# Performance work log

Measured on AMD Instinct MI355X. Metric: run time of the kernel, lower is better.

Reference implementation:

```python
import jax, jax.numpy as jnp
import numpy as np

B = 8192
IN = 2048
H = 2048


def setup_inputs() -> dict:
    key = jax.random.key(0)
    ks = jax.random.split(key, 6)
    stdv = 1.0 / np.sqrt(H)
    return {
        "x": jax.random.normal(ks[0], (B, IN), dtype=jnp.float32),
        "h_prev": jax.random.normal(ks[1], (B, H), dtype=jnp.float32),
        "c_prev": jax.random.normal(ks[2], (B, H), dtype=jnp.float32),
        "weight_ih": jax.random.normal(ks[3], (4 * H, IN), dtype=jnp.float32) * stdv,
        "weight_hh": jax.random.normal(ks[4], (4 * H, H), dtype=jnp.float32) * stdv,
        "bias": jax.random.normal(ks[5], (4 * H,), dtype=jnp.float32) * stdv,
    }


def reference(x, h_prev, c_prev, weight_ih, weight_hh, bias):
    # gates: [B, 4H] = x @ W_ih^T + h_prev @ W_hh^T + b
    gates = x @ weight_ih.T + h_prev @ weight_hh.T + bias
    i, f, j, o = jnp.split(gates, 4, axis=1)
    i = jax.nn.sigmoid(i)
    f = jax.nn.sigmoid(f)
    o = jax.nn.sigmoid(o)
    j = jnp.tanh(j)
    # cap_input_gate=True: input gate capped by (1 - f)
    c = f * c_prev + jnp.minimum(1.0 - f, i) * j
    h = o * jnp.tanh(c)
    return (h, c)
```

## Files before the change

kernel.cpp:

```cpp
#include <hip/hip_runtime.h>

#define DEVI __device__ __forceinline__

typedef __attribute__((ext_vector_type(8))) __bf16 bf16x8;
typedef __attribute__((ext_vector_type(4))) float floatx4;

constexpr int Bsz = 8192;
constexpr int Hd  = 2048;
constexpr int INd = 2048;
constexpr int N1  = Bsz * INd;

DEVI unsigned short f2bf_rne(float f) {
  unsigned int u = __float_as_uint(f);
  u += 0x7FFFu + ((u >> 16) & 1u);
  return (unsigned short)(u >> 16);
}

__global__ void cvt4(const float* __restrict__ s0, const float* __restrict__ s1,
                     const float* __restrict__ s2, const float* __restrict__ s3,
                     unsigned short* __restrict__ dst) {
  const float* src = (blockIdx.y == 0) ? s0 : (blockIdx.y == 1) ? s1
                   : (blockIdx.y == 2) ? s2 : s3;
  unsigned short* out = dst + (size_t)blockIdx.y * N1;
  const int nv = N1 / 4;
  for (int i = blockIdx.x * blockDim.x + threadIdx.x; i < nv;
       i += gridDim.x * blockDim.x) {
    float4 v = ((const float4*)src)[i];
    ushort4 o;
    o.x = f2bf_rne(v.x); o.y = f2bf_rne(v.y);
    o.z = f2bf_rne(v.z); o.w = f2bf_rne(v.w);
    ((ushort4*)out)[i] = o;
  }
}

DEVI void gload_lds16(const void* g, void* l) {
  __builtin_amdgcn_global_load_lds(
      (const __attribute__((address_space(1))) void*)g,
      (__attribute__((address_space(3))) void*)l, 16, 0, 0);
}

DEVI float sigm(float x) { return 1.0f / (1.0f + __expf(-x)); }

__global__ __launch_bounds__(512, 2) void lstm_gemm(
    const unsigned short* __restrict__ ws,
    const float* __restrict__ bias,
    const float* __restrict__ c_prev,
    float* __restrict__ out_h,
    float* __restrict__ out_c) {
  __shared__ __align__(16) unsigned short sm[4 * 256 * 64];
  char* smc = (char*)sm;

  const unsigned short* xb  = ws;
  const unsigned short* hb  = ws + (size_t)N1;
  const unsigned short* wih = ws + (size_t)2 * N1;
  const unsigned short* whh = ws + (size_t)3 * N1;

  const int tid  = threadIdx.x;
  const int lane = tid & 63;
  const int wid  = tid >> 6;
  const int wm   = wid >> 2, wn = wid & 3;
  const int lr   = lane & 15, lk = lane >> 4;
  const int lr8  = lane >> 3;
  const int swc  = ((lane & 7) ^ lr8) * 8;

  const int wg = blockIdx.x;
  const int x8 = wg & 7;
  const int lc = wg >> 3;
  const int bc = (x8 & 3) * 8 + (lc & 7);
  const int rb = ((x8 >> 2) * 16 + (lc >> 3)) * 256;

  unsigned int aOff[2][2], bOff[2][2];
#pragma unroll
  for (int h = 0; h < 2; ++h)
#pragma unroll
    for (int j = 0; j < 2; ++j) {
      const int arow = rb + h * 128 + j * 64 + wid * 8 + lr8;
      aOff[h][j] = (unsigned)arow * 2048u + (unsigned)swc;
      const int c  = h * 128 + j * 64 + wid * 8 + lr8;
      const int cf = c >> 4, ce = c & 15;
      const int gate = (cf & 1) | ((cf >> 2) & 2);
      const int hch  = (cf >> 1) & 3;
      const int brow = gate * 2048 + bc * 64 + hch * 16 + ce;
      bOff[h][j] = (unsigned)brow * 2048u + (unsigned)swc;
    }

  floatx4 acc[2][4][2][2];
#pragma unroll
  for (int a = 0; a < 2; ++a)
#pragma unroll
    for (int b = 0; b < 4; ++b)
#pragma unroll
      for (int c = 0; c < 2; ++c)
#pragma unroll
        for (int d = 0; d < 2; ++d)
          acc[a][b][c][d] = (floatx4){0.f, 0.f, 0.f, 0.f};

#define STAGE_A(ts, h) {                                                      \
    const int bs_ = (ts) & 1;                                                 \
    const unsigned short* s_ = (((ts) < 32) ? xb : hb) + (((ts) & 31) * 64);  \
    gload_lds16(s_ + aOff[h][0], smc + bs_ * 32768 + ((h) * 128 + wid * 8) * 128);        \
    gload_lds16(s_ + aOff[h][1], smc + bs_ * 32768 + ((h) * 128 + 64 + wid * 8) * 128); }
#define STAGE_B(ts, h) {                                                      \
    const int bs_ = (ts) & 1;                                                 \
    const unsigned short* s_ = (((ts) < 32) ? wih : whh) + (((ts) & 31) * 64);\
    gload_lds16(s_ + bOff[h][0], smc + 65536 + bs_ * 32768 + ((h) * 128 + wid * 8) * 128);        \
    gload_lds16(s_ + bOff[h][1], smc + 65536 + bs_ * 32768 + ((h) * 128 + 64 + wid * 8) * 128); }

#define LDA(DST, QM)                                                          \
  _Pragma("unroll") for (int mr = 0; mr < 4; ++mr)                            \
    _Pragma("unroll") for (int s = 0; s < 2; ++s) {                           \
      const int row  = (QM) * 128 + wm * 64 + mr * 16 + lr;                   \
      const int phys = (s * 4 + lk) ^ (row & 7);                              \
      DST[mr][s] = *(const bf16x8*)(Ab + row * 128 + phys * 16); }
#define LDB(DST, QN)                                                          \
  _Pragma("unroll") for (int nc = 0; nc < 2; ++nc)                            \
    _Pragma("unroll") for (int s = 0; s < 2; ++s) {                           \
      const int row  = ((QN) * 8 + wn * 2 + nc) * 16 + lr;                    \
      const int phys = (s * 4 + lk) ^ (row & 7);                              \
      DST[nc][s] = *(const bf16x8*)(Bb + row * 128 + phys * 16); }
#define MFMA16(QM, QN, AF, BG)                                                \
  __builtin_amdgcn_s_setprio(1);                                              \
  _Pragma("unroll") for (int mr = 0; mr < 4; ++mr)                            \
    _Pragma("unroll") for (int nc = 0; nc < 2; ++nc)                          \
      _Pragma("unroll") for (int s = 0; s < 2; ++s)                           \
        acc[QM][mr][QN][nc] = __builtin_amdgcn_mfma_f32_16x16x32_bf16(        \
            AF[mr][s], BG[nc][s], acc[QM][mr][QN][nc], 0, 0, 0);              \
  __builtin_amdgcn_s_setprio(0);
#define BAR  asm volatile("s_barrier" ::: "memory")
#define LGK0 do { asm volatile("s_waitcnt lgkmcnt(0)" ::: "memory");          \
                  __builtin_amdgcn_sched_barrier(0); } while (0)

#define KTILE(BETA, S1, S2, S3, S4, W4) {                                     \
    const char* Ab = smc + (BETA) * 32768;                                    \
    const char* Bb = smc + 65536 + (BETA) * 32768;                            \
    bf16x8 afA[4][2], afB[4][2], bg[2][2];                                    \
    LDA(afA, 0); LDB(bg, 0); S1;                                              \
    asm volatile("s_waitcnt lgkmcnt(8)" ::: "memory");                        \
    BAR; LGK0; MFMA16(0, 0, afA, bg); BAR;                                    \
    LDA(afB, 1); S2;                                                          \
    BAR; LGK0; MFMA16(1, 0, afB, bg); BAR;                                    \
    LDB(bg, 1); S3;                                                           \
    BAR; LGK0; MFMA16(1, 1, afB, bg); BAR;                                    \
    LDA(afA, 0); S4; W4;                                                      \
    BAR; LGK0; MFMA16(0, 1, afA, bg); BAR;                                    \
  }
#define VM4  asm volatile("s_waitcnt vmcnt(4)" ::: "memory")
#define VM0  asm volatile("s_waitcnt vmcnt(0)" ::: "memory")
#define NOP  (void)0

  STAGE_B(0, 0); STAGE_A(0, 1); STAGE_B(0, 1);
  STAGE_A(0, 0); STAGE_B(1, 0); STAGE_A(1, 1);
  VM4;
  BAR;

  for (int t = 0; t < 62; ++t) {
    KTILE(t & 1, STAGE_B(t + 1, 1), STAGE_A(t + 1, 0),
          STAGE_B(t + 2, 0), STAGE_A(t + 2, 1), VM4);
  }
  KTILE(0, STAGE_B(63, 1), STAGE_A(63, 0), NOP, NOP, VM0);
  KTILE(1, NOP, NOP, NOP, NOP, NOP);

  const int hcol = bc * 64 + wn * 16 + lr;
  const float b_i = bias[hcol];
  const float b_f = bias[2048 + hcol];
  const float b_j = bias[4096 + hcol];
  const float b_o = bias[6144 + hcol];
#pragma unroll
  for (int qm = 0; qm < 2; ++qm)
#pragma unroll
    for (int mr = 0; mr < 4; ++mr)
#pragma unroll
      for (int r = 0; r < 4; ++r) {
        const int row = rb + qm * 128 + wm * 64 + mr * 16 + lk * 4 + r;
        const float gi = acc[qm][mr][0][0][r] + b_i;
        const float gf = acc[qm][mr][0][1][r] + b_f;
        const float gj = acc[qm][mr][1][0][r] + b_j;
        const float go = acc[qm][mr][1][1][r] + b_o;
        const float iv = sigm(gi);
        const float fv = sigm(gf);
        const float jv = tanhf(gj);
        const float ov = sigm(go);
        const size_t idx = (size_t)row * 2048 + hcol;
        const float cp = c_prev[idx];
        const float cv = fv * cp + fminf(1.0f - fv, iv) * jv;
        out_h[idx] = ov * tanhf(cv);
        out_c[idx] = cv;
      }
}

extern "C" void kernel_launch(void* const* d_in, const int* in_sizes, int n_in,
                              void* d_out, int out_size, void* d_ws, size_t ws_size,
                              hipStream_t stream) {
  const float* x      = (const float*)d_in[0];
  const float* h_prev = (const float*)d_in[1];
  const float* c_prev = (const float*)d_in[2];
  const float* w_ih   = (const float*)d_in[3];
  const float* w_hh   = (const float*)d_in[4];
  const float* bias   = (const float*)d_in[5];

  float* out_h = (float*)d_out;
  float* out_c = out_h + (size_t)Bsz * Hd;
  unsigned short* wsb = (unsigned short*)d_ws;

  dim3 cgrid(2048, 4);
  cvt4<<<cgrid, 256, 0, stream>>>(x, h_prev, w_ih, w_hh, wsb);

  lstm_gemm<<<1024, 512, 0, stream>>>(wsb, bias, c_prev, out_h, out_c);
}
```

Before: 599.8 us.

## Switch LSTM GEMM to 32x32x16 MFMA with swapped operands and vectorized epilogue

Replaces the 16x16x32 bf16 MFMA tiling with 32x32x16 MFMAs, with the weights as the A operand and activations as B. Weight rows are re-permuted so each lane's 16 accumulator outputs cover the i/f/j/o gates for 4 contiguous hidden columns. This allows float4 loads of bias and c_prev and float4 stores of h and c. The k-tile schedule is also simplified: the lgkmcnt waits and per-phase double barriers are dropped, which cuts sync overhead but relies on the compiler to insert correct LDS waits.

```diff
diff --git a/kernel.cpp b/kernel.cpp
--- a/kernel.cpp
+++ b/kernel.cpp
@@ -3,7 +3,7 @@
 #define DEVI __device__ __forceinline__
 
 typedef __attribute__((ext_vector_type(8))) __bf16 bf16x8;
-typedef __attribute__((ext_vector_type(4))) float floatx4;
+typedef __attribute__((ext_vector_type(16))) float floatx16;
 
 constexpr int Bsz = 8192;
 constexpr int Hd  = 2048;
@@ -58,8 +58,9 @@
   const int tid  = threadIdx.x;
   const int lane = tid & 63;
   const int wid  = tid >> 6;
-  const int wm   = wid >> 2, wn = wid & 3;
-  const int lr   = lane & 15, lk = lane >> 4;
+  const int ww   = wid >> 2;
+  const int wb   = wid & 3;
+  const int l31  = lane & 31, l5 = lane >> 5;
   const int lr8  = lane >> 3;
   const int swc  = ((lane & 7) ^ lr8) * 8;
 
@@ -76,24 +77,20 @@
     for (int j = 0; j < 2; ++j) {
       const int arow = rb + h * 128 + j * 64 + wid * 8 + lr8;
       aOff[h][j] = (unsigned)arow * 2048u + (unsigned)swc;
-      const int c  = h * 128 + j * 64 + wid * 8 + lr8;
-      const int cf = c >> 4, ce = c & 15;
-      const int gate = (cf & 1) | ((cf >> 2) & 2);
-      const int hch  = (cf >> 1) & 3;
-      const int brow = gate * 2048 + bc * 64 + hch * 16 + ce;
-      bOff[h][j] = (unsigned)brow * 2048u + (unsigned)swc;
+      const int wr = h * 128 + j * 64 + wid * 8 + lr8;
+      const int wrow = ((wr >> 3) & 3) * 2048 + bc * 64 + (wr >> 5) * 8 + (wr & 7);
+      bOff[h][j] = (unsigned)wrow * 2048u + (unsigned)swc;
     }
 
-  floatx4 acc[2][4][2][2];
+  floatx16 acc[2][2][2];
 #pragma unroll
   for (int a = 0; a < 2; ++a)
 #pragma unroll
-    for (int b = 0; b < 4; ++b)
+    for (int b = 0; b < 2; ++b)
 #pragma unroll
       for (int c = 0; c < 2; ++c)
 #pragma unroll
-        for (int d = 0; d < 2; ++d)
-          acc[a][b][c][d] = (floatx4){0.f, 0.f, 0.f, 0.f};
+        for (int e = 0; e < 16; ++e) acc[a][b][c][e] = 0.f;
 
 #define STAGE_A(ts, h) {                                                      \
     const int bs_ = (ts) & 1;                                                 \
@@ -106,86 +103,88 @@
     gload_lds16(s_ + bOff[h][0], smc + 65536 + bs_ * 32768 + ((h) * 128 + wid * 8) * 128);        \
     gload_lds16(s_ + bOff[h][1], smc + 65536 + bs_ * 32768 + ((h) * 128 + 64 + wid * 8) * 128); }
 
-#define LDA(DST, QM)                                                          \
-  _Pragma("unroll") for (int mr = 0; mr < 4; ++mr)                            \
-    _Pragma("unroll") for (int s = 0; s < 2; ++s) {                           \
-      const int row  = (QM) * 128 + wm * 64 + mr * 16 + lr;                   \
-      const int phys = (s * 4 + lk) ^ (row & 7);                              \
-      DST[mr][s] = *(const bf16x8*)(Ab + row * 128 + phys * 16); }
-#define LDB(DST, QN)                                                          \
-  _Pragma("unroll") for (int nc = 0; nc < 2; ++nc)                            \
-    _Pragma("unroll") for (int s = 0; s < 2; ++s) {                           \
-      const int row  = ((QN) * 8 + wn * 2 + nc) * 16 + lr;                    \
-      const int phys = (s * 4 + lk) ^ (row & 7);                              \
-      DST[nc][s] = *(const bf16x8*)(Bb + row * 128 + phys * 16); }
-#define MFMA16(QM, QN, AF, BG)                                                \
+#define LDW(DST, QW)                                                          \
+  _Pragma("unroll") for (int mrw = 0; mrw < 2; ++mrw)                         \
+    _Pragma("unroll") for (int ks = 0; ks < 4; ++ks) {                        \
+      const int row  = (QW) * 128 + ww * 64 + mrw * 32 + l31;                 \
+      const int phys = (ks * 2 + l5) ^ (row & 7);                             \
+      DST[mrw][ks] = *(const bf16x8*)(Bb + row * 128 + phys * 16); }
+#define LDX(DST, QB)                                                          \
+  _Pragma("unroll") for (int ks = 0; ks < 4; ++ks) {                          \
+      const int row  = (QB) * 128 + wb * 32 + l31;                            \
+      const int phys = (ks * 2 + l5) ^ (row & 7);                             \
+      DST[ks] = *(const bf16x8*)(Ab + row * 128 + phys * 16); }
+#define MM(QW, QB, WF, XF)                                                    \
   __builtin_amdgcn_s_setprio(1);                                              \
-  _Pragma("unroll") for (int mr = 0; mr < 4; ++mr)                            \
-    _Pragma("unroll") for (int nc = 0; nc < 2; ++nc)                          \
-      _Pragma("unroll") for (int s = 0; s < 2; ++s)                           \
-        acc[QM][mr][QN][nc] = __builtin_amdgcn_mfma_f32_16x16x32_bf16(        \
-            AF[mr][s], BG[nc][s], acc[QM][mr][QN][nc], 0, 0, 0);              \
+  _Pragma("unroll") for (int mrw = 0; mrw < 2; ++mrw)                         \
+    _Pragma("unroll") for (int ks = 0; ks < 4; ++ks)                          \
+      acc[QW][mrw][QB] = __builtin_amdgcn_mfma_f32_32x32x16_bf16(             \
+          WF[mrw][ks], XF[ks], acc[QW][mrw][QB], 0, 0, 0);                    \
   __builtin_amdgcn_s_setprio(0);
 #define BAR  asm volatile("s_barrier" ::: "memory")
-#define LGK0 do { asm volatile("s_waitcnt lgkmcnt(0)" ::: "memory");          \
-                  __builtin_amdgcn_sched_barrier(0); } while (0)
-
-#define KTILE(BETA, S1, S2, S3, S4, W4) {                                     \
-    const char* Ab = smc + (BETA) * 32768;                                    \
-    const char* Bb = smc + 65536 + (BETA) * 32768;                            \
-    bf16x8 afA[4][2], afB[4][2], bg[2][2];                                    \
-    LDA(afA, 0); LDB(bg, 0); S1;                                              \
-    asm volatile("s_waitcnt lgkmcnt(8)" ::: "memory");                        \
-    BAR; LGK0; MFMA16(0, 0, afA, bg); BAR;                                    \
-    LDA(afB, 1); S2;                                                          \
-    BAR; LGK0; MFMA16(1, 0, afB, bg); BAR;                                    \
-    LDB(bg, 1); S3;                                                           \
-    BAR; LGK0; MFMA16(1, 1, afB, bg); BAR;                                    \
-    LDA(afA, 0); S4; W4;                                                      \
-    BAR; LGK0; MFMA16(0, 1, afA, bg); BAR;                                    \
-  }
 #define VM4  asm volatile("s_waitcnt vmcnt(4)" ::: "memory")
 #define VM0  asm volatile("s_waitcnt vmcnt(0)" ::: "memory")
 #define NOP  (void)0
 
-  STAGE_B(0, 0); STAGE_A(0, 1); STAGE_B(0, 1);
-  STAGE_A(0, 0); STAGE_B(1, 0); STAGE_A(1, 1);
+#define KTILE(BETA, S1, S2a, S2b, S3, W4) {                                   \
+    const char* Ab = smc + (BETA) * 32768;                                    \
+    const char* Bb = smc + 65536 + (BETA) * 32768;                            \
+    bf16x8 wf[2][4], xf0[4], xf1[4];                                          \
+    LDW(wf, 0); LDX(xf0, 0); S1;                                              \
+    MM(0, 0, wf, xf0); BAR;                                                   \
+    LDX(xf1, 1); S2a; S2b;                                                    \
+    MM(0, 1, wf, xf1); BAR;                                                   \
+    LDW(wf, 1); S3;                                                           \
+    MM(1, 1, wf, xf1); BAR;                                                   \
+    LDX(xf0, 0);                                                              \
+    MM(1, 0, wf, xf0); W4; BAR;                                               \
+  }
+
+  STAGE_A(0, 0); STAGE_A(0, 1); STAGE_B(0, 0); STAGE_B(0, 1);
+  STAGE_B(1, 0); STAGE_A(1, 1);
   VM4;
   BAR;
 
   for (int t = 0; t < 62; ++t) {
-    KTILE(t & 1, STAGE_B(t + 1, 1), STAGE_A(t + 1, 0),
+    KTILE(t & 1, STAGE_A(t + 1, 0), STAGE_B(t + 1, 1),
           STAGE_B(t + 2, 0), STAGE_A(t + 2, 1), VM4);
   }
-  KTILE(0, STAGE_B(63, 1), STAGE_A(63, 0), NOP, NOP, VM0);
+  KTILE(0, STAGE_A(63, 0), STAGE_B(63, 1), NOP, NOP, VM0);
   KTILE(1, NOP, NOP, NOP, NOP, NOP);
 
-  const int hcol = bc * 64 + wn * 16 + lr;
-  const float b_i = bias[hcol];
-  const float b_f = bias[2048 + hcol];
-  const float b_j = bias[4096 + hcol];
-  const float b_o = bias[6144 + hcol];
-#pragma unroll
-  for (int qm = 0; qm < 2; ++qm)
-#pragma unroll
-    for (int mr = 0; mr < 4; ++mr)
-#pragma unroll
-      for (int r = 0; r < 4; ++r) {
-        const int row = rb + qm * 128 + wm * 64 + mr * 16 + lk * 4 + r;
-        const float gi = acc[qm][mr][0][0][r] + b_i;
-        const float gf = acc[qm][mr][0][1][r] + b_f;
-        const float gj = acc[qm][mr][1][0][r] + b_j;
-        const float go = acc[qm][mr][1][1][r] + b_o;
-        const float iv = sigm(gi);
-        const float fv = sigm(gf);
-        const float jv = tanhf(gj);
-        const float ov = sigm(go);
-        const size_t idx = (size_t)row * 2048 + hcol;
-        const float cp = c_prev[idx];
-        const float cv = fv * cp + fminf(1.0f - fv, iv) * jv;
-        out_h[idx] = ov * tanhf(cv);
-        out_c[idx] = cv;
+#pragma unroll
+  for (int qw = 0; qw < 2; ++qw)
+#pragma unroll
+    for (int mrw = 0; mrw < 2; ++mrw) {
+      const int hb4 = bc * 64 + (qw * 4 + ww * 2 + mrw) * 8 + l5 * 4;
+      const float4 bi4 = *(const float4*)&bias[hb4];
+      const float4 bf4 = *(const float4*)&bias[2048 + hb4];
+      const float4 bj4 = *(const float4*)&bias[4096 + hb4];
+      const float4 bo4 = *(const float4*)&bias[6144 + hb4];
+#pragma unroll
+      for (int qb = 0; qb < 2; ++qb) {
+        const int brow = rb + qb * 128 + wb * 32 + l31;
+        const size_t base = (size_t)brow * 2048 + hb4;
+        const float4 cp = *(const float4*)&c_prev[base];
+        float4 hv, cv;
+#pragma unroll
+        for (int q = 0; q < 4; ++q) {
+          const float gi = acc[qw][mrw][qb][q]      + ((const float*)&bi4)[q];
+          const float gf = acc[qw][mrw][qb][4 + q]  + ((const float*)&bf4)[q];
+          const float gj = acc[qw][mrw][qb][8 + q]  + ((const float*)&bj4)[q];
+          const float go = acc[qw][mrw][qb][12 + q] + ((const float*)&bo4)[q];
+          const float iv = sigm(gi);
+          const float fv = sigm(gf);
+          const float jv = tanhf(gj);
+          const float ov = sigm(go);
+          const float cq = fv * ((const float*)&cp)[q] + fminf(1.0f - fv, iv) * jv;
+          ((float*)&cv)[q] = cq;
+          ((float*)&hv)[q] = ov * tanhf(cq);
+        }
+        *(float4*)&out_h[base] = hv;
+        *(float4*)&out_c[base] = cv;
       }
+    }
 }
 
 extern "C" void kernel_launch(void* const* d_in, const int* in_sizes, int n_in,
```

After: 640.0 us. 1.07x slower.
